# Performance work log

Hardware: AMD Instinct MI355X
Metric: run time of the kernel (lower is better)

The kernel has to match this reference:

```python
import jax, jax.numpy as jnp
import numpy as np

B, L, D_MODEL, N_HEADS = 2, 2048, 1024, 16
D_HEAD = D_MODEL // N_HEADS


def setup_inputs() -> dict:
    key = jax.random.key(0)
    k0, k1, k2 = jax.random.split(key, 3)
    x = jax.random.normal(k0, (B, L, D_MODEL), dtype=jnp.float32)
    qkv_w = jax.random.normal(k1, (3 * D_MODEL, D_MODEL), dtype=jnp.float32) * 0.02
    qkv_b = jnp.zeros((3 * D_MODEL,), dtype=jnp.float32)
    o_w = jax.random.normal(k2, (D_MODEL, D_MODEL), dtype=jnp.float32) * 0.02
    o_b = jnp.zeros((D_MODEL,), dtype=jnp.float32)
    attn_mask = jnp.ones((B, 1, L, L), dtype=jnp.int32)  # 1 = visible
    return {"x": x, "qkv_w": qkv_w, "qkv_b": qkv_b, "o_w": o_w, "o_b": o_b, "attn_mask": attn_mask}


def _rope(x, sin, cos):
    half = x.shape[-1] // 2
    x1, x2 = x[..., :half], x[..., half:]
    return jnp.concatenate([x1 * cos - x2 * sin, x1 * sin + x2 * cos], axis=-1)


def reference(x, qkv_w, qkv_b, o_w, o_b, attn_mask):
    Bx, Lx, D = x.shape
    H, Dh = N_HEADS, D // N_HEADS
    qkv = x @ qkv_w.T + qkv_b                          # (B, L, 3D)
    qkv = qkv.reshape(Bx, Lx, 3, H, Dh).transpose(2, 0, 3, 1, 4)  # (3, B, H, L, Dh)
    q, k, v = qkv[0], qkv[1], qkv[2]
    # RoPE: freq_i = 1/10000^(2i/Dh) over first half of head dim
    half = Dh // 2
    freq = 1.0 / (10000.0 ** (2.0 * jnp.arange(half, dtype=jnp.float32) / Dh))
    t = jnp.arange(Lx, dtype=jnp.float32)
    freqs = t[:, None] * freq[None, :]                 # (L, half)
    sin, cos = jnp.sin(freqs), jnp.cos(freqs)
    q, k = _rope(q, sin, cos), _rope(k, sin, cos)
    scores = jnp.einsum('bhqd,bhkd->bhqk', q, k) / jnp.sqrt(jnp.float32(Dh))
    causal = jnp.tril(jnp.ones((Lx, Lx), dtype=bool))  # (L, L)
    neg_inf = jnp.float32(-jnp.inf)
    scores = jnp.where(causal[None, None], scores, neg_inf)
    scores = jnp.where(attn_mask == 0, neg_inf, scores)
    probs = jax.nn.softmax(scores, axis=-1)
    ctx = jnp.einsum('bhqk,bhkd->bhqd', probs, v)      # (B, H, L, Dh)
    ctx = ctx.transpose(0, 2, 1, 3).reshape(Bx, Lx, D)
    return ctx @ o_w.T + o_b
```

## Files before the change

kernel.cpp:

```cpp
#include <hip/hip_runtime.h>

#define Bz 2
#define Lz 2048
#define Dm 1024
#define Hh 16
#define Dh 64

typedef float f32x4 __attribute__((ext_vector_type(4)));
typedef short bf16x8 __attribute__((ext_vector_type(8)));
typedef short bf16x4 __attribute__((ext_vector_type(4)));

typedef __attribute__((address_space(1))) void GV;
typedef __attribute__((address_space(3))) void LV;

#if defined(__has_builtin)
#if __has_builtin(__builtin_amdgcn_mfma_f32_16x16x16bf16_1k)
#define HAVE_MFMA16 1
#endif
#if __has_builtin(__builtin_amdgcn_exp2f)
#define EXP2(x) __builtin_amdgcn_exp2f(x)
#endif
#endif
#ifndef EXP2
#define EXP2(x) exp2f(x)
#endif

#define QSCALE 0.18033688011112042f

__device__ __forceinline__ short f2bf(float f) {
    union { float f; unsigned int u; } c; c.f = f;
    unsigned int u = c.u;
    unsigned int r = (u + 0x7fffu + ((u >> 16) & 1u)) >> 16;
    return (short)r;
}

__global__ __launch_bounds__(256) void cvt_all(
    const float* __restrict__ x, const float* __restrict__ qw,
    const float* __restrict__ ow, unsigned short* __restrict__ xb,
    unsigned short* __restrict__ qwb, unsigned short* __restrict__ owb,
    float2* __restrict__ tab)
{
    int u = blockIdx.x * 256 + threadIdx.x;
    if (u < 1048576) {
        const float* in; unsigned short* out; int off;
        if (u < 524288)       { in = x;  out = xb;  off = u; }
        else if (u < 917504)  { in = qw; out = qwb; off = u - 524288; }
        else                  { in = ow; out = owb; off = u - 917504; }
        const float4 f0 = *reinterpret_cast<const float4*>(in + (size_t)off * 8);
        const float4 f1 = *reinterpret_cast<const float4*>(in + (size_t)off * 8 + 4);
        bf16x8 o;
        o[0] = f2bf(f0.x); o[1] = f2bf(f0.y); o[2] = f2bf(f0.z); o[3] = f2bf(f0.w);
        o[4] = f2bf(f1.x); o[5] = f2bf(f1.y); o[6] = f2bf(f1.z); o[7] = f2bf(f1.w);
        *reinterpret_cast<bf16x8*>(out + (size_t)off * 8) = o;
    } else {
        int t = u - 1048576;
        int l = t >> 5, d = t & 31;
        float fr = exp2f(-(float)d * 0.41524101186092029f);
        float ang = (float)l * fr;
        tab[t] = make_float2(sinf(ang), cosf(ang));
    }
}

template <int MODE, int TN>
__global__ __launch_bounds__(256, 3) void gemm_bt_bf16(
    const unsigned short* __restrict__ A, const unsigned short* __restrict__ W,
    const float* __restrict__ bias, void* __restrict__ Cv,
    unsigned short* __restrict__ Vt, const float2* __restrict__ tab, int N, int K)
{
    constexpr int NB = (TN == 128) ? 4 : 2;
    constexpr int SR = 36;
    __shared__ __align__(16) unsigned short At[2][128 * SR];
    __shared__ __align__(16) unsigned short Wt[2][TN * SR];

    const int t = threadIdx.x;
    const int lane = t & 63;
    const int wv = t >> 6;
    const int wm = wv >> 1, wn = wv & 1;
    const int r = lane & 15, q4 = lane >> 4;
    const int m0 = blockIdx.y * 128;
    const int n0 = blockIdx.x * TN;

    const int ar = t >> 1, ac = (t & 1) * 16;
    const int wr = (TN == 128) ? (t >> 1) : (t >> 2);
    const int wc = (TN == 128) ? ((t & 1) * 16) : ((t & 3) * 8);

    const unsigned short* Ap = A + (size_t)(m0 + ar) * K + ac;
    const unsigned short* Wp = W + (size_t)(n0 + wr) * K + wc;

    f32x4 acc[4][NB] = {};

    bf16x8 sa0, sa1, sw0, sw1;
    sa0 = *reinterpret_cast<const bf16x8*>(Ap);
    sa1 = *reinterpret_cast<const bf16x8*>(Ap + 8);
    sw0 = *reinterpret_cast<const bf16x8*>(Wp);
    if constexpr (TN == 128) sw1 = *reinterpret_cast<const bf16x8*>(Wp + 8);

    *reinterpret_cast<bf16x8*>(&At[0][ar * SR + ac]) = sa0;
    *reinterpret_cast<bf16x8*>(&At[0][ar * SR + ac + 8]) = sa1;
    *reinterpret_cast<bf16x8*>(&Wt[0][wr * SR + wc]) = sw0;
    if constexpr (TN == 128) *reinterpret_cast<bf16x8*>(&Wt[0][wr * SR + wc + 8]) = sw1;
    __syncthreads();

    const int NIT = K / 32;
    int buf = 0;
    for (int it = 0; it < NIT; ++it) {
        const bool more = (it + 1 < NIT);
        if (more) {
            const int k = (it + 1) * 32;
            sa0 = *reinterpret_cast<const bf16x8*>(Ap + k);
            sa1 = *reinterpret_cast<const bf16x8*>(Ap + k + 8);
            sw0 = *reinterpret_cast<const bf16x8*>(Wp + k);
            if constexpr (TN == 128) sw1 = *reinterpret_cast<const bf16x8*>(Wp + k + 8);
        }

        bf16x8 af[4], bfr[NB];
#pragma unroll
        for (int mi = 0; mi < 4; mi++)
            af[mi] = *reinterpret_cast<bf16x8*>(&At[buf][(wm * 64 + mi * 16 + r) * SR + q4 * 8]);
#pragma unroll
        for (int ni = 0; ni < NB; ni++)
            bfr[ni] = *reinterpret_cast<bf16x8*>(&Wt[buf][(wn * (TN / 2) + ni * 16 + r) * SR + q4 * 8]);
#pragma unroll
        for (int mi = 0; mi < 4; mi++)
#pragma unroll
            for (int ni = 0; ni < NB; ni++)
                acc[mi][ni] = __builtin_amdgcn_mfma_f32_16x16x32_bf16(
                    af[mi], bfr[ni], acc[mi][ni], 0, 0, 0);

        if (more) {
            const int nb = buf ^ 1;
            *reinterpret_cast<bf16x8*>(&At[nb][ar * SR + ac]) = sa0;
            *reinterpret_cast<bf16x8*>(&At[nb][ar * SR + ac + 8]) = sa1;
            *reinterpret_cast<bf16x8*>(&Wt[nb][wr * SR + wc]) = sw0;
            if constexpr (TN == 128) *reinterpret_cast<bf16x8*>(&Wt[nb][wr * SR + wc + 8]) = sw1;
            __syncthreads();
            buf = nb;
        }
    }

    if constexpr (MODE == 2) {
        const int colbase = n0 + wn * 64;
        if (colbase >= 2048) {
            const int hh = (colbase - 2048) >> 6;
#pragma unroll
            for (int mi = 0; mi < 4; mi++) {
                const int row0 = m0 + wm * 64 + mi * 16 + q4 * 4;
                const int bb = row0 >> 11;
                const int lc = (row0 & 2047) >> 2;
#pragma unroll
                for (int ni = 0; ni < 4; ni++) {
                    const int dd = ni * 16 + r;
                    const float bv = bias[colbase + ni * 16 + r];
                    ushort4 st;
                    st.x = (unsigned short)f2bf(acc[mi][ni][0] + bv);
                    st.y = (unsigned short)f2bf(acc[mi][ni][1] + bv);
                    st.z = (unsigned short)f2bf(acc[mi][ni][2] + bv);
                    st.w = (unsigned short)f2bf(acc[mi][ni][3] + bv);
                    *reinterpret_cast<ushort4*>(
                        &Vt[((size_t)((bb * 16 + hh) * 512 + lc)) * 256 + dd * 4]) = st;
                }
            }
        } else {
            const float qs = (colbase < 1024) ? QSCALE : 1.0f;
            unsigned short* qko = (unsigned short*)Cv;
#pragma unroll
            for (int np = 0; np < 2; np++) {
                const int d = np * 16 + r;
                const float2 rot = tab[32 + d];
                const float blo = bias[colbase + np * 16 + r];
                const float bhi = bias[colbase + np * 16 + r + 32];
#pragma unroll
                for (int mi = 0; mi < 4; mi++) {
                    const int row0 = m0 + wm * 64 + mi * 16 + q4 * 4;
                    const int l0 = row0 & 2047;
                    const float2 sc = tab[l0 * 32 + d];
                    float s = sc.x, c = sc.y;
#pragma unroll
                    for (int reg = 0; reg < 4; reg++) {
                        float x1 = acc[mi][np][reg] + blo;
                        float x2 = acc[mi][np + 2][reg] + bhi;
                        float olo = (x1 * c - x2 * s) * qs;
                        float ohi = (x1 * s + x2 * c) * qs;
                        size_t rowoff = (size_t)(row0 + reg) * 2048 + colbase + np * 16 + r;
                        qko[rowoff] = (unsigned short)f2bf(olo);
                        qko[rowoff + 32] = (unsigned short)f2bf(ohi);
                        float s2 = s * rot.y + c * rot.x;
                        c = c * rot.y - s * rot.x;
                        s = s2;
                    }
                }
            }
        }
    } else {
#pragma unroll
        for (int mi = 0; mi < 4; mi++)
#pragma unroll
            for (int ni = 0; ni < NB; ni++) {
                int col = n0 + wn * (TN / 2) + ni * 16 + r;
                float bv = bias[col];
#pragma unroll
                for (int reg = 0; reg < 4; reg++) {
                    int row = m0 + wm * 64 + mi * 16 + q4 * 4 + reg;
                    ((float*)Cv)[(size_t)row * N + col] = acc[mi][ni][reg] + bv;
                }
            }
    }
}

__global__ __launch_bounds__(256) void attn_kernel(
    const unsigned short* __restrict__ qk, const unsigned short* __restrict__ Vt,
    unsigned short* __restrict__ ctx)
{
    const int n = blockIdx.x;
    const int bh = (n & 7) | (((n >> 3) & 3) << 3);
    const int qi = 31 - (n >> 5);
    const int b = bh >> 4, h = bh & 15;
    const int w = threadIdx.x >> 6;
    const int lane = threadIdx.x & 63;
    const int r = lane & 15, q4 = lane >> 4;

    __shared__ __align__(16) unsigned short Kbuf[64 * 64];
    __shared__ __align__(16) unsigned short Vbuf[64 * 64];
#ifndef HAVE_MFMA16
    __shared__ __align__(16) unsigned short Pl[4][16][72];
#endif

    const unsigned short* kg =
        qk + ((size_t)(b * Lz + w * 16 + (lane >> 3))) * 2048 + 1024 + h * 64
           + (((lane & 7) ^ (lane >> 3)) * 8);
    const unsigned short* vg =
        Vt + ((size_t)(bh * 512 + w * 4 + (lane >> 5))) * 256 + (lane & 31) * 8;

    const int qb = qi * 64;
    const int wq = qb + w * 16;

    const unsigned short* qptr = qk + ((size_t)(b * Lz + wq + r)) * 2048 + h * 64;
    bf16x8 qf[2];
    qf[0] = *reinterpret_cast<const bf16x8*>(qptr + q4 * 8);
    qf[1] = *reinterpret_cast<const bf16x8*>(qptr + 32 + q4 * 8);

    f32x4 o[4] = {};
    float l_i = 0.f;

    const int ntiles = qi + 1;
    for (int it = 0; it < ntiles; ++it) {
        const int k0 = it * 64;
        __syncthreads();
#pragma unroll
        for (int half = 0; half < 2; half++) {
            __builtin_amdgcn_global_load_lds(
                (GV*)(kg + (size_t)(k0 + half * 8) * 2048),
                (LV*)&Kbuf[(w * 16 + half * 8) * 64], 16, 0, 0);
            __builtin_amdgcn_global_load_lds(
                (GV*)(vg + (size_t)((k0 >> 2) + half * 2) * 256),
                (LV*)&Vbuf[(w * 4 + half * 2) * 256], 16, 0, 0);
        }
        __syncthreads();

        f32x4 S[4] = {};
#pragma unroll
        for (int ns = 0; ns < 4; ns++)
#pragma unroll
            for (int ks = 0; ks < 2; ks++) {
                bf16x8 kf = *reinterpret_cast<bf16x8*>(
                    &Kbuf[(ns * 16 + r) * 64 + (((ks * 4 + q4) ^ (r & 7)) * 8)]);
                S[ns] = __builtin_amdgcn_mfma_f32_16x16x32_bf16(kf, qf[ks], S[ns], 0, 0, 0);
            }

        if (k0 + 63 > wq) {
#pragma unroll
            for (int ns = 0; ns < 4; ns++) {
                int key = k0 + ns * 16 + q4 * 4;
#pragma unroll
                for (int reg = 0; reg < 4; reg++)
                    if (key + reg > wq + r) S[ns][reg] = -1e30f;
            }
        }

        float sum = 0.f;
#pragma unroll
        for (int ns = 0; ns < 4; ns++)
#pragma unroll
            for (int reg = 0; reg < 4; reg++) {
                S[ns][reg] = EXP2(S[ns][reg]);
                sum += S[ns][reg];
            }
        sum += __shfl_xor(sum, 16);
        sum += __shfl_xor(sum, 32);
        l_i += sum;

#ifdef HAVE_MFMA16
        bf16x4 pf[4];
#pragma unroll
        for (int ns = 0; ns < 4; ns++) {
            bf16x4 p;
#pragma unroll
            for (int reg = 0; reg < 4; reg++) p[reg] = f2bf(S[ns][reg]);
            pf[ns] = p;
        }
#pragma unroll
        for (int ns = 0; ns < 4; ns++)
#pragma unroll
            for (int dt = 0; dt < 4; dt++) {
                bf16x4 vf = *reinterpret_cast<bf16x4*>(
                    &Vbuf[((ns * 4 + q4) * 64 + dt * 16 + r) * 4]);
                o[dt] = __builtin_amdgcn_mfma_f32_16x16x16bf16_1k(vf, pf[ns], o[dt], 0, 0, 0);
            }
#else
#pragma unroll
        for (int ns = 0; ns < 4; ns++)
#pragma unroll
            for (int reg = 0; reg < 4; reg++)
                Pl[w][r][ns * 16 + q4 * 4 + reg] = (unsigned short)f2bf(S[ns][reg]);
#pragma unroll
        for (int ks32 = 0; ks32 < 2; ks32++) {
            bf16x8 pf8 = *reinterpret_cast<bf16x8*>(&Pl[w][r][ks32 * 32 + q4 * 8]);
#pragma unroll
            for (int dt = 0; dt < 4; dt++) {
                bf16x4 vlo = *reinterpret_cast<bf16x4*>(
                    &Vbuf[((ks32 * 8 + q4 * 2) * 64 + dt * 16 + r) * 4]);
                bf16x4 vhi = *reinterpret_cast<bf16x4*>(
                    &Vbuf[((ks32 * 8 + q4 * 2 + 1) * 64 + dt * 16 + r) * 4]);
                bf16x8 vf8;
                vf8[0] = vlo[0]; vf8[1] = vlo[1]; vf8[2] = vlo[2]; vf8[3] = vlo[3];
                vf8[4] = vhi[0]; vf8[5] = vhi[1]; vf8[6] = vhi[2]; vf8[7] = vhi[3];
                o[dt] = __builtin_amdgcn_mfma_f32_16x16x32_bf16(vf8, pf8, o[dt], 0, 0, 0);
            }
        }
#endif
    }

    float rl = 1.0f / l_i;
    unsigned short* cp =
        ctx + ((size_t)(b * Lz + wq + r)) * Dm + h * 64 + q4 * 4;
#pragma unroll
    for (int dt = 0; dt < 4; dt++) {
        ushort4 st;
        st.x = (unsigned short)f2bf(o[dt][0] * rl);
        st.y = (unsigned short)f2bf(o[dt][1] * rl);
        st.z = (unsigned short)f2bf(o[dt][2] * rl);
        st.w = (unsigned short)f2bf(o[dt][3] * rl);
        *reinterpret_cast<ushort4*>(cp + dt * 16) = st;
    }
}

extern "C" void kernel_launch(void* const* d_in, const int* in_sizes, int n_in,
                              void* d_out, int out_size, void* d_ws, size_t ws_size,
                              hipStream_t stream)
{
    const float* x     = (const float*)d_in[0];
    const float* qkv_w = (const float*)d_in[1];
    const float* qkv_b = (const float*)d_in[2];
    const float* o_w   = (const float*)d_in[3];
    const float* o_b   = (const float*)d_in[4];

    char* ws = (char*)d_ws;
    unsigned short* xb   = (unsigned short*)(ws);
    unsigned short* qwb  = (unsigned short*)(ws + ( 8u << 20));
    unsigned short* owb  = (unsigned short*)(ws + (14u << 20));
    unsigned short* qkb  = (unsigned short*)(ws + (16u << 20));
    unsigned short* Vtb  = (unsigned short*)(ws + (32u << 20));
    unsigned short* ctxb = (unsigned short*)(ws + (40u << 20));
    float2* tab          = (float2*)(ws + (48u << 20));
    float* out = (float*)d_out;

    cvt_all<<<4352, 256, 0, stream>>>(x, qkv_w, o_w, xb, qwb, owb, tab);
    gemm_bt_bf16<2, 128><<<dim3(24, 32), 256, 0, stream>>>(
        xb, qwb, qkv_b, qkb, Vtb, tab, 3072, 1024);
    attn_kernel<<<1024, 256, 0, stream>>>(qkb, Vtb, ctxb);
    gemm_bt_bf16<0, 64><<<dim3(16, 32), 256, 0, stream>>>(
        ctxb, owb, o_b, out, nullptr, nullptr, 1024, 1024);
}
```

Baseline: 198.8 us.

## Double-buffer attention K/V tiles and deepen GEMM global prefetch

The attention kernel swaps its direct global-to-LDS loads, which ran between two barriers, for register prefetch of the next K/V tile into a second LDS buffer, leaving one barrier per tile. The GEMM loop is unrolled by two and keeps two k-steps of global loads in flight in registers. The aim is to hide global load latency behind MFMA work and cut barrier stalls. The cost is more registers and double the LDS in attention, which may lower occupancy.

```diff
diff --git a/kernel.cpp b/kernel.cpp
--- a/kernel.cpp
+++ b/kernel.cpp
@@ -10,9 +10,6 @@
 typedef short bf16x8 __attribute__((ext_vector_type(8)));
 typedef short bf16x4 __attribute__((ext_vector_type(4)));
 
-typedef __attribute__((address_space(1))) void GV;
-typedef __attribute__((address_space(3))) void LV;
-
 #if defined(__has_builtin)
 #if __has_builtin(__builtin_amdgcn_mfma_f32_16x16x16bf16_1k)
 #define HAVE_MFMA16 1
@@ -32,6 +29,13 @@
     unsigned int u = c.u;
     unsigned int r = (u + 0x7fffu + ((u >> 16) & 1u)) >> 16;
     return (short)r;
+}
+
+__device__ __forceinline__ bf16x8 ld8(const unsigned short* p) {
+    return *reinterpret_cast<const bf16x8*>(p);
+}
+__device__ __forceinline__ void st8(unsigned short* p, bf16x8 v) {
+    *reinterpret_cast<bf16x8*>(p) = v;
 }
 
 __global__ __launch_bounds__(256) void cvt_all(
@@ -89,52 +93,61 @@
 
     f32x4 acc[4][NB] = {};
 
-    bf16x8 sa0, sa1, sw0, sw1;
-    sa0 = *reinterpret_cast<const bf16x8*>(Ap);
-    sa1 = *reinterpret_cast<const bf16x8*>(Ap + 8);
-    sw0 = *reinterpret_cast<const bf16x8*>(Wp);
-    if constexpr (TN == 128) sw1 = *reinterpret_cast<const bf16x8*>(Wp + 8);
-
-    *reinterpret_cast<bf16x8*>(&At[0][ar * SR + ac]) = sa0;
-    *reinterpret_cast<bf16x8*>(&At[0][ar * SR + ac + 8]) = sa1;
-    *reinterpret_cast<bf16x8*>(&Wt[0][wr * SR + wc]) = sw0;
-    if constexpr (TN == 128) *reinterpret_cast<bf16x8*>(&Wt[0][wr * SR + wc + 8]) = sw1;
+    bf16x8 sa0[2], sa1[2], sw0[2], sw1[2];
+    sa0[0] = ld8(Ap);      sa1[0] = ld8(Ap + 8);
+    sw0[0] = ld8(Wp);      if constexpr (TN == 128) sw1[0] = ld8(Wp + 8);
+    sa0[1] = ld8(Ap + 32); sa1[1] = ld8(Ap + 40);
+    sw0[1] = ld8(Wp + 32); if constexpr (TN == 128) sw1[1] = ld8(Wp + 40);
+
+    st8(&At[0][ar * SR + ac], sa0[0]);
+    st8(&At[0][ar * SR + ac + 8], sa1[0]);
+    st8(&Wt[0][wr * SR + wc], sw0[0]);
+    if constexpr (TN == 128) st8(&Wt[0][wr * SR + wc + 8], sw1[0]);
     __syncthreads();
 
-    const int NIT = K / 32;
-    int buf = 0;
-    for (int it = 0; it < NIT; ++it) {
-        const bool more = (it + 1 < NIT);
-        if (more) {
-            const int k = (it + 1) * 32;
-            sa0 = *reinterpret_cast<const bf16x8*>(Ap + k);
-            sa1 = *reinterpret_cast<const bf16x8*>(Ap + k + 8);
-            sw0 = *reinterpret_cast<const bf16x8*>(Wp + k);
-            if constexpr (TN == 128) sw1 = *reinterpret_cast<const bf16x8*>(Wp + k + 8);
-        }
-
+    auto compute = [&](int b) {
         bf16x8 af[4], bfr[NB];
 #pragma unroll
         for (int mi = 0; mi < 4; mi++)
-            af[mi] = *reinterpret_cast<bf16x8*>(&At[buf][(wm * 64 + mi * 16 + r) * SR + q4 * 8]);
+            af[mi] = ld8(&At[b][(wm * 64 + mi * 16 + r) * SR + q4 * 8]);
 #pragma unroll
         for (int ni = 0; ni < NB; ni++)
-            bfr[ni] = *reinterpret_cast<bf16x8*>(&Wt[buf][(wn * (TN / 2) + ni * 16 + r) * SR + q4 * 8]);
+            bfr[ni] = ld8(&Wt[b][(wn * (TN / 2) + ni * 16 + r) * SR + q4 * 8]);
 #pragma unroll
         for (int mi = 0; mi < 4; mi++)
 #pragma unroll
             for (int ni = 0; ni < NB; ni++)
                 acc[mi][ni] = __builtin_amdgcn_mfma_f32_16x16x32_bf16(
                     af[mi], bfr[ni], acc[mi][ni], 0, 0, 0);
-
-        if (more) {
-            const int nb = buf ^ 1;
-            *reinterpret_cast<bf16x8*>(&At[nb][ar * SR + ac]) = sa0;
-            *reinterpret_cast<bf16x8*>(&At[nb][ar * SR + ac + 8]) = sa1;
-            *reinterpret_cast<bf16x8*>(&Wt[nb][wr * SR + wc]) = sw0;
-            if constexpr (TN == 128) *reinterpret_cast<bf16x8*>(&Wt[nb][wr * SR + wc + 8]) = sw1;
+    };
+
+    const int NIT = K / 32;
+    for (int it = 0; it < NIT; it += 2) {
+        if (it + 2 < NIT) {
+            const int k = (it + 2) * 32;
+            sa0[0] = ld8(Ap + k); sa1[0] = ld8(Ap + k + 8);
+            sw0[0] = ld8(Wp + k); if constexpr (TN == 128) sw1[0] = ld8(Wp + k + 8);
+        }
+        compute(0);
+        {
+            st8(&At[1][ar * SR + ac], sa0[1]);
+            st8(&At[1][ar * SR + ac + 8], sa1[1]);
+            st8(&Wt[1][wr * SR + wc], sw0[1]);
+            if constexpr (TN == 128) st8(&Wt[1][wr * SR + wc + 8], sw1[1]);
             __syncthreads();
-            buf = nb;
+        }
+        if (it + 3 < NIT) {
+            const int k = (it + 3) * 32;
+            sa0[1] = ld8(Ap + k); sa1[1] = ld8(Ap + k + 8);
+            sw0[1] = ld8(Wp + k); if constexpr (TN == 128) sw1[1] = ld8(Wp + k + 8);
+        }
+        compute(1);
+        if (it + 2 < NIT) {
+            st8(&At[0][ar * SR + ac], sa0[0]);
+            st8(&At[0][ar * SR + ac + 8], sa1[0]);
+            st8(&Wt[0][wr * SR + wc], sw0[0]);
+            if constexpr (TN == 128) st8(&Wt[0][wr * SR + wc + 8], sw1[0]);
+            __syncthreads();
         }
     }
 
@@ -219,8 +232,8 @@
     const int lane = threadIdx.x & 63;
     const int r = lane & 15, q4 = lane >> 4;
 
-    __shared__ __align__(16) unsigned short Kbuf[64 * 64];
-    __shared__ __align__(16) unsigned short Vbuf[64 * 64];
+    __shared__ __align__(16) unsigned short Kbuf[2][64 * 64];
+    __shared__ __align__(16) unsigned short Vbuf[2][64 * 64];
 #ifndef HAVE_MFMA16
     __shared__ __align__(16) unsigned short Pl[4][16][72];
 #endif
@@ -230,40 +243,50 @@
            + (((lane & 7) ^ (lane >> 3)) * 8);
     const unsigned short* vg =
         Vt + ((size_t)(bh * 512 + w * 4 + (lane >> 5))) * 256 + (lane & 31) * 8;
+    const int kd0 = (w * 16 + 0) * 64 + lane * 8;
+    const int kd1 = (w * 16 + 8) * 64 + lane * 8;
+    const int vd0 = (w * 4 + 0) * 256 + lane * 8;
+    const int vd1 = (w * 4 + 2) * 256 + lane * 8;
 
     const int qb = qi * 64;
     const int wq = qb + w * 16;
 
     const unsigned short* qptr = qk + ((size_t)(b * Lz + wq + r)) * 2048 + h * 64;
     bf16x8 qf[2];
-    qf[0] = *reinterpret_cast<const bf16x8*>(qptr + q4 * 8);
-    qf[1] = *reinterpret_cast<const bf16x8*>(qptr + 32 + q4 * 8);
+    qf[0] = ld8(qptr + q4 * 8);
+    qf[1] = ld8(qptr + 32 + q4 * 8);
 
     f32x4 o[4] = {};
     float l_i = 0.f;
+
+    bf16x8 kr0 = ld8(kg);
+    bf16x8 kr1 = ld8(kg + (size_t)8 * 2048);
+    bf16x8 vr0 = ld8(vg);
+    bf16x8 vr1 = ld8(vg + 2 * 256);
+    st8(&Kbuf[0][kd0], kr0); st8(&Kbuf[0][kd1], kr1);
+    st8(&Vbuf[0][vd0], vr0); st8(&Vbuf[0][vd1], vr1);
+    __syncthreads();
 
     const int ntiles = qi + 1;
     for (int it = 0; it < ntiles; ++it) {
         const int k0 = it * 64;
-        __syncthreads();
-#pragma unroll
-        for (int half = 0; half < 2; half++) {
-            __builtin_amdgcn_global_load_lds(
-                (GV*)(kg + (size_t)(k0 + half * 8) * 2048),
-                (LV*)&Kbuf[(w * 16 + half * 8) * 64], 16, 0, 0);
-            __builtin_amdgcn_global_load_lds(
-                (GV*)(vg + (size_t)((k0 >> 2) + half * 2) * 256),
-                (LV*)&Vbuf[(w * 4 + half * 2) * 256], 16, 0, 0);
-        }
-        __syncthreads();
+        const bool more = (it + 1 < ntiles);
+        if (more) {
+            const int kn = k0 + 64;
+            kr0 = ld8(kg + (size_t)kn * 2048);
+            kr1 = ld8(kg + (size_t)(kn + 8) * 2048);
+            vr0 = ld8(vg + (kn >> 2) * 256);
+            vr1 = ld8(vg + ((kn >> 2) + 2) * 256);
+        }
+        const unsigned short* Kb = Kbuf[it & 1];
+        const unsigned short* Vb = Vbuf[it & 1];
 
         f32x4 S[4] = {};
 #pragma unroll
         for (int ns = 0; ns < 4; ns++)
 #pragma unroll
             for (int ks = 0; ks < 2; ks++) {
-                bf16x8 kf = *reinterpret_cast<bf16x8*>(
-                    &Kbuf[(ns * 16 + r) * 64 + (((ks * 4 + q4) ^ (r & 7)) * 8)]);
+                bf16x8 kf = ld8(&Kb[(ns * 16 + r) * 64 + (((ks * 4 + q4) ^ (r & 7)) * 8)]);
                 S[ns] = __builtin_amdgcn_mfma_f32_16x16x32_bf16(kf, qf[ks], S[ns], 0, 0, 0);
             }
 
@@ -302,8 +325,8 @@
         for (int ns = 0; ns < 4; ns++)
 #pragma unroll
             for (int dt = 0; dt < 4; dt++) {
-                bf16x4 vf = *reinterpret_cast<bf16x4*>(
-                    &Vbuf[((ns * 4 + q4) * 64 + dt * 16 + r) * 4]);
+                bf16x4 vf = *reinterpret_cast<const bf16x4*>(
+                    &Vb[((ns * 4 + q4) * 64 + dt * 16 + r) * 4]);
                 o[dt] = __builtin_amdgcn_mfma_f32_16x16x16bf16_1k(vf, pf[ns], o[dt], 0, 0, 0);
             }
 #else
@@ -317,10 +340,10 @@
             bf16x8 pf8 = *reinterpret_cast<bf16x8*>(&Pl[w][r][ks32 * 32 + q4 * 8]);
 #pragma unroll
             for (int dt = 0; dt < 4; dt++) {
-                bf16x4 vlo = *reinterpret_cast<bf16x4*>(
-                    &Vbuf[((ks32 * 8 + q4 * 2) * 64 + dt * 16 + r) * 4]);
-                bf16x4 vhi = *reinterpret_cast<bf16x4*>(
-                    &Vbuf[((ks32 * 8 + q4 * 2 + 1) * 64 + dt * 16 + r) * 4]);
+                bf16x4 vlo = *reinterpret_cast<const bf16x4*>(
+                    &Vb[((ks32 * 8 + q4 * 2) * 64 + dt * 16 + r) * 4]);
+                bf16x4 vhi = *reinterpret_cast<const bf16x4*>(
+                    &Vb[((ks32 * 8 + q4 * 2 + 1) * 64 + dt * 16 + r) * 4]);
                 bf16x8 vf8;
                 vf8[0] = vlo[0]; vf8[1] = vlo[1]; vf8[2] = vlo[2]; vf8[3] = vlo[3];
                 vf8[4] = vhi[0]; vf8[5] = vhi[1]; vf8[6] = vhi[2]; vf8[7] = vhi[3];
@@ -328,6 +351,14 @@
             }
         }
 #endif
+
+        if (more) {
+            unsigned short* Kn = Kbuf[(it + 1) & 1];
+            unsigned short* Vn = Vbuf[(it + 1) & 1];
+            st8(&Kn[kd0], kr0); st8(&Kn[kd1], kr1);
+            st8(&Vn[vd0], vr0); st8(&Vn[vd1], vr1);
+            __syncthreads();
+        }
     }
 
     float rl = 1.0f / l_i;
```

Measured after the change: 337.7 us. +69.8%, slower.
